# Performance work log

Hardware: AMD Instinct MI355X
Metric: run time of the kernel (lower is better)

Reference implementation:

```python
import jax, jax.numpy as jnp
import numpy as np

PAD = 1
DIL = 1
K = 9  # 3x3 kernel points


def conv2d(x, w, b):
    # standard NCHW conv, stride 1, padding PAD, dilation DIL
    y = jax.lax.conv_general_dilated(
        x, w, window_strides=(1, 1), padding=[(PAD, PAD), (PAD, PAD)],
        rhs_dilation=(DIL, DIL), dimension_numbers=('NCHW', 'OIHW', 'NCHW'))
    return y + b[None, :, None, None]


def deform_conv(x, offset, w):
    # x: [B,C,H,W], offset: [B,2K,H,W] (y at 2k, x at 2k+1), w: [O,C,3,3]
    B, C, H, W = x.shape
    O = w.shape[0]
    off = offset.reshape(B, K, 2, H, W)
    ky = jnp.repeat(jnp.arange(3), 3).astype(x.dtype)  # [K]
    kx = jnp.tile(jnp.arange(3), 3).astype(x.dtype)    # [K]
    base_h = jnp.arange(H, dtype=x.dtype) - PAD
    base_w = jnp.arange(W, dtype=x.dtype) - PAD
    # sampling positions [B,K,H,W]
    py = base_h[None, None, :, None] + (ky * DIL)[None, :, None, None] + off[:, :, 0]
    px = base_w[None, None, None, :] + (kx * DIL)[None, :, None, None] + off[:, :, 1]
    y0 = jnp.floor(py)
    x0 = jnp.floor(px)
    wy = py - y0
    wx = px - x0

    def gather(yi, xi):
        yc = jnp.clip(yi, 0, H - 1).astype(jnp.int32)
        xc = jnp.clip(xi, 0, W - 1).astype(jnp.int32)
        valid = ((yi >= 0) & (yi <= H - 1) & (xi >= 0) & (xi <= W - 1)).astype(x.dtype)
        # per-batch fancy gather -> [B,C,K,H,W]
        v = jax.vmap(lambda xb, yb, xbb: xb[:, yb, xbb])(x, yc, xc)
        return v * valid[:, None]

    v00 = gather(y0, x0)
    v01 = gather(y0, x0 + 1)
    v10 = gather(y0 + 1, x0)
    v11 = gather(y0 + 1, x0 + 1)
    a = (1 - wy)[:, None]; b_ = wy[:, None]
    c = (1 - wx)[:, None]; d = wx[:, None]
    samp = v00 * a * c + v01 * a * d + v10 * b_ * c + v11 * b_ * d  # [B,C,K,H,W]
    return jnp.einsum('bckhw,ock->bohw', samp, w.reshape(O, C, K))


def layer(x, w_off, b_off, w):
    offset = conv2d(x, w_off, b_off)
    return jax.nn.relu(deform_conv(x, offset, w))


def setup_inputs() -> dict:
    key = jax.random.key(0)
    ks = jax.random.split(key, 10)
    B, C, H, W = 4, 256, 96, 96
    inp = {"x": jax.random.normal(ks[0], (B, C, H, W), jnp.float32)}
    s = 1.0 / np.sqrt(C * 9)  # kaiming-ish scale for deform weights
    for i in range(3):
        inp[f"w_off{i}"] = jax.random.normal(ks[1 + 3 * i], (2 * K, C, 3, 3), jnp.float32) * 0.01
        inp[f"b_off{i}"] = jnp.zeros((2 * K,), jnp.float32)
        inp[f"w{i}"] = jax.random.normal(ks[3 + 3 * i], (C, C, 3, 3), jnp.float32) * s
    return inp


def reference(x, w_off0, b_off0, w0, w_off1, b_off1, w1, w_off2, b_off2, w2):
    for (wo, bo, w) in ((w_off0, b_off0, w0), (w_off1, b_off1, w1), (w_off2, b_off2, w2)):
        x = layer(x, wo, bo, w)
    return x
```

## Files before the change

kernel.cpp:

```cpp
#include <hip/hip_runtime.h>

#define Hc 96
#define Wc 96
#define Cc 256
#define Bc 4
#define KK 9
#define HW 9216
#define PIX 36864
#define CK 2304

typedef _Float16 f16;
typedef __attribute__((ext_vector_type(4))) _Float16 f16x4;
typedef __attribute__((ext_vector_type(8))) _Float16 f16x8;
typedef __attribute__((ext_vector_type(4))) float f32x4;

__device__ __forceinline__ int clampi(int v, int lo, int hi) {
    return v < lo ? lo : (v > hi ? hi : v);
}

#define SB() __builtin_amdgcn_sched_barrier(0)

__global__ __launch_bounds__(256) void nhwc_prep_kernel(
    const float* __restrict__ x0, f16* __restrict__ x16)
{
    __shared__ float st[64][65];
    const int hw0 = blockIdx.x * 64;
    const int c0  = blockIdx.y * 64;
    const int b   = blockIdx.z;
    const int tid = threadIdx.x;
    const int a = tid & 63, r = tid >> 6;
#pragma unroll
    for (int it = 0; it < 16; ++it) {
        int cl = it * 4 + r;
        st[cl][a] = x0[((size_t)(b * Cc + c0 + cl)) * HW + hw0 + a];
    }
    __syncthreads();
#pragma unroll
    for (int it = 0; it < 16; ++it) {
        int hwl = it * 4 + r;
        x16[((size_t)(b * HW + hw0 + hwl)) * Cc + c0 + a] = (f16)st[a][hwl];
    }
}

__global__ __launch_bounds__(256) void wprep_kernel(
    const float* __restrict__ w, const float* __restrict__ w_off,
    f16* __restrict__ wT2, f16* __restrict__ woffT)
{
    int b = blockIdx.x;
    if (b < 2304) {
        int u = b * 256 + threadIdx.x;
        int c = u & 255, o = (u >> 8) & 255, k = u >> 16;
        wT2[u] = (f16)w[(o * Cc + c) * KK + k];
    } else {
        int u = (b - 2304) * 256 + threadIdx.x;
        int c = u & 255, j = (u >> 8) & 31, k = u >> 13;
        float v = (j < 18) ? w_off[((size_t)j * Cc + c) * KK + k] : 0.f;
        woffT[u] = (f16)v;
    }
}

__device__ __forceinline__ void store_tap(int k, int h, int w, float offy, float offx,
    int p, int4* __restrict__ idx4t, float4* __restrict__ wt4t)
{
    float py = (float)(h - 1 + k / 3) + offy;
    float px = (float)(w - 1 + k % 3) + offx;
    float y0f = floorf(py), x0f = floorf(px);
    float wy = py - y0f, wx = px - x0f;
    int iy0 = (int)y0f, ix0 = (int)x0f;
    float vy0 = (y0f >= 0.f && y0f <= 95.f) ? 1.f : 0.f;
    float vy1 = (y0f + 1.f >= 0.f && y0f + 1.f <= 95.f) ? 1.f : 0.f;
    float vx0 = (x0f >= 0.f && x0f <= 95.f) ? 1.f : 0.f;
    float vx1 = (x0f + 1.f >= 0.f && x0f + 1.f <= 95.f) ? 1.f : 0.f;
    int cy0 = clampi(iy0, 0, 95), cy1 = clampi(iy0 + 1, 0, 95);
    int cx0 = clampi(ix0, 0, 95), cx1 = clampi(ix0 + 1, 0, 95);
    idx4t[(size_t)k * PIX + p] = make_int4(cy0 * Wc + cx0, cy0 * Wc + cx1,
                                           cy1 * Wc + cx0, cy1 * Wc + cx1);
    wt4t[(size_t)k * PIX + p] = make_float4((1.f - wy) * (1.f - wx) * vy0 * vx0,
                                            (1.f - wy) * wx * vy0 * vx1,
                                            wy * (1.f - wx) * vy1 * vx0,
                                            wy * wx * vy1 * vx1);
}

__global__ __launch_bounds__(256) void conv_off_mfma_kernel(
    const f16* __restrict__ x16, const f16* __restrict__ woffT,
    const float* __restrict__ b_off,
    int4* __restrict__ idx4t, float4* __restrict__ wt4t)
{
    __shared__ __align__(16) f16 s_a[2][32 * 32];
    __shared__ __align__(16) f16 s_b[2][64 * 32];
    const int bid = blockIdx.x;
    const int swz = (bid & 7) * 72 + (bid >> 3);
    const int p0 = swz * 64;
    const int imgb = (p0 / HW) * HW;
    const int tid = threadIdx.x, lane = tid & 63, wid = tid >> 6;
    const int wm = wid >> 1, wn = wid & 1;
    const int qa = ((lane >> 4) ^ ((lane >> 1) & 3)) * 8;
    const int arow = tid >> 3, acb = tid & 7;
    const int adst = arow * 32 + (((acb >> 1) ^ ((arow >> 1) & 3)) * 8) + (acb & 1) * 4;
    const int ps = tid >> 2, cg = tid & 3;
    const int bdst = ps * 32 + ((cg ^ ((ps >> 1) & 3)) * 8);
    const int hwp = p0 + ps - imgb;
    const int hp = hwp / Wc, wp = hwp - hp * Wc;

#define CLOAD(q, aD, bD) do {                                                  \
    int p2_ = (q) > 71 ? 71 : (q);                                             \
    int k2_ = p2_ >> 3, c2_ = p2_ & 7;                                         \
    int ky_ = k2_ / 3, kx_ = k2_ - ky_ * 3;                                    \
    int yy_ = hp + ky_ - 1, xx_ = wp + kx_ - 1;                                \
    bool v_ = (yy_ >= 0 && yy_ < Hc && xx_ >= 0 && xx_ < Wc);                  \
    aD = *(const f16x4*)(woffT + ((size_t)(k2_ * 32 + arow)) * Cc + c2_ * 32 + acb * 4); \
    f16x8 t_ = {0, 0, 0, 0, 0, 0, 0, 0};                                       \
    if (v_) t_ = *(const f16x8*)(x16 + ((size_t)(imgb + yy_ * Wc + xx_)) * Cc + c2_ * 32 + cg * 8); \
    bD = t_;                                                                   \
} while (0)

    f32x4 acc[2];
    acc[0] = (f32x4){0.f, 0.f, 0.f, 0.f};
    acc[1] = (f32x4){0.f, 0.f, 0.f, 0.f};

    f16x4 aR0, aR1;
    f16x8 bR0, bR1;
    CLOAD(0, aR0, bR0);
    CLOAD(1, aR1, bR1);
    *(f16x4*)&s_a[0][adst] = aR0;
    *(f16x8*)&s_b[0][bdst] = bR0;
    asm volatile("s_waitcnt lgkmcnt(0)" ::: "memory"); SB();
    __builtin_amdgcn_s_barrier(); SB();

#define CBODY(p, aCur, bCur, aNxt, bNxt, bc, bn) do {                          \
    f16x8 af = *(const f16x8*)&s_a[bc][(wm * 16 + (lane & 15)) * 32 + qa];     \
    f16x8 bf0 = *(const f16x8*)&s_b[bc][(wn * 32 + (lane & 15)) * 32 + qa];    \
    f16x8 bf1 = *(const f16x8*)&s_b[bc][(wn * 32 + 16 + (lane & 15)) * 32 + qa];\
    CLOAD((p) + 2, aCur, bCur);                                                \
    acc[0] = __builtin_amdgcn_mfma_f32_16x16x32_f16(af, bf0, acc[0], 0, 0, 0); \
    acc[1] = __builtin_amdgcn_mfma_f32_16x16x32_f16(af, bf1, acc[1], 0, 0, 0); \
    *(f16x4*)&s_a[bn][adst] = aNxt;                                            \
    *(f16x8*)&s_b[bn][bdst] = bNxt;                                            \
    asm volatile("s_waitcnt lgkmcnt(0)" ::: "memory"); SB();                   \
    __builtin_amdgcn_s_barrier(); SB();                                        \
} while (0)

    for (int p = 0; p < 72; p += 2) {
        CBODY(p,     aR0, bR0, aR1, bR1, 0, 1);
        CBODY(p + 1, aR1, bR1, aR0, bR0, 1, 0);
    }

    const int g = lane >> 4;
#pragma unroll
    for (int ni = 0; ni < 2; ++ni) {
        const int p = p0 + wn * 32 + ni * 16 + (lane & 15);
        const int hwq = p - imgb;
        const int hq = hwq / Wc, wq = hwq - hq * Wc;
        if (wm == 0) {
            store_tap(2 * g,     hq, wq, acc[ni][0] + b_off[4 * g],
                                         acc[ni][1] + b_off[4 * g + 1], p, idx4t, wt4t);
            store_tap(2 * g + 1, hq, wq, acc[ni][2] + b_off[4 * g + 2],
                                         acc[ni][3] + b_off[4 * g + 3], p, idx4t, wt4t);
        } else if (g == 0) {
            store_tap(8, hq, wq, acc[ni][0] + b_off[16],
                                 acc[ni][1] + b_off[17], p, idx4t, wt4t);
        }
    }
#undef CLOAD
#undef CBODY
}

__global__ __launch_bounds__(768, 3) void deform_mfma_kernel(
    const f16* __restrict__ x16, const f16* __restrict__ wT2,
    const int4* __restrict__ idx4t, const float4* __restrict__ wt4t,
    f16* __restrict__ o16, float* __restrict__ oN, int last)
{
    __shared__ __align__(16) f16 s_w[2][2][8192];
    __shared__ __align__(16) f16 s_s[2][2][4608];

    const int bid = blockIdx.x;
    const int swz = (bid & 7) * 32 + (bid >> 3);
    const int p0 = swz * 144;
    const int imgb = (p0 / HW) * HW;
    const int tid = threadIdx.x, lane = tid & 63, wid = tid >> 6;
    const int wo = wid & 3, wp = wid >> 2;
    const bool sampler = (wid < 9);
    const int ps = tid >> 2, cg = tid & 3;
    const int qa = ((lane >> 4) ^ ((lane >> 1) & 3)) * 8;
    const int qs = (cg ^ ((ps >> 1) & 3)) * 8;
    const f16* xb = x16 + (size_t)imgb * Cc;
    const int wlo = (tid >> 2) * Cc + ((tid & 3) ^ ((tid >> 3) & 3)) * 8;
    const int wds = tid * 8;

#define ISSUE_W(kt, cq, h, nb) do {                                            \
    const f16* g0_ = wT2 + wlo + ((size_t)((kt) * 256)) * Cc + (cq) * 64 + (h) * 32; \
    __builtin_amdgcn_global_load_lds(                                          \
        (const __attribute__((address_space(1))) void*)g0_,                    \
        (__attribute__((address_space(3))) void*)&s_w[nb][h][wds], 16, 0, 0);  \
    if (wid >= 8) {                                                            \
        const f16* g1_ = wT2 + wlo + ((size_t)((kt) * 256 + 64)) * Cc + (cq) * 64 + (h) * 32; \
        __builtin_amdgcn_global_load_lds(                                      \
            (const __attribute__((address_space(1))) void*)g1_,                \
            (__attribute__((address_space(3))) void*)&s_w[nb][h][2048 + wds], 16, 0, 0); \
    }                                                                          \
} while (0)

#define ISSUE_C(dst, idv, co) do {                                             \
    (dst)[0] = *(const f16x8*)(xb + (size_t)(idv).x * Cc + (co) + cg * 8);     \
    (dst)[1] = *(const f16x8*)(xb + (size_t)(idv).y * Cc + (co) + cg * 8);     \
    (dst)[2] = *(const f16x8*)(xb + (size_t)(idv).z * Cc + (co) + cg * 8);     \
    (dst)[3] = *(const f16x8*)(xb + (size_t)(idv).w * Cc + (co) + cg * 8);     \
} while (0)

#define BLEND_WRITE(src, wvv, h, nb) do {                                      \
    f16x8 sv_ = (src)[0] * (f16)(wvv).x + (src)[1] * (f16)(wvv).y              \
              + (src)[2] * (f16)(wvv).z + (src)[3] * (f16)(wvv).w;             \
    *(f16x8*)&s_s[nb][h][ps * 32 + qs] = sv_;                                  \
} while (0)

    f32x4 acc[4][3];
#pragma unroll
    for (int mi = 0; mi < 4; ++mi)
#pragma unroll
        for (int ni = 0; ni < 3; ++ni) acc[mi][ni] = (f32x4){0.f, 0.f, 0.f, 0.f};

    f16x8 c4a[4], c4b[4];
    int4 id;
    float4 wv;
    int4 idN;
    float4 wvN;
    if (sampler) {
        id = idx4t[p0 + ps];
        wv = wt4t[p0 + ps];
    }

    ISSUE_W(0, 0, 0, 0);
    ISSUE_W(0, 0, 1, 0);
    SB();
    if (sampler) {
        ISSUE_C(c4a, id, 0);
        ISSUE_C(c4b, id, 32);
        BLEND_WRITE(c4a, wv, 0, 0);
        BLEND_WRITE(c4b, wv, 1, 0);
        ISSUE_C(c4a, id, 64);
        ISSUE_C(c4b, id, 96);
        asm volatile("s_waitcnt lgkmcnt(0)" ::: "memory"); SB();
        if (wid == 8) {
            asm volatile("s_waitcnt vmcnt(8)" ::: "memory"); SB();
        }
    } else {
        asm volatile("s_waitcnt vmcnt(0)" ::: "memory"); SB();
    }
    __builtin_amdgcn_s_barrier(); SB();

    for (int k = 0; k < 9; ++k) {
        const int kn = (k < 8) ? k + 1 : 8;
#pragma unroll
        for (int ch = 0; ch < 4; ++ch) {
            const int bb = ch & 1, nb = bb ^ 1;
            f16x8 bf0[3], bf1[3];
#pragma unroll
            for (int ni = 0; ni < 3; ++ni) {
                bf0[ni] = *(const f16x8*)&s_s[bb][0][(wp * 48 + ni * 16 + (lane & 15)) * 32 + qa];
                bf1[ni] = *(const f16x8*)&s_s[bb][1][(wp * 48 + ni * 16 + (lane & 15)) * 32 + qa];
            }
            if (sampler) {
                if (ch == 1) {
                    idN = idx4t[(size_t)kn * PIX + p0 + ps];
                    wvN = wt4t[(size_t)kn * PIX + p0 + ps];
                }
                ISSUE_W((ch == 3) ? kn : k, (ch + 1) & 3, 0, nb);
                ISSUE_W((ch == 3) ? kn : k, (ch + 1) & 3, 1, nb);
                SB();
                {
                    const float4 wvu = (ch == 3) ? wvN : wv;
                    const int4 idu = (ch >= 2) ? idN : id;
                    const int co2 = ((ch + 2) & 3) * 64;
                    BLEND_WRITE(c4a, wvu, 0, nb);
                    ISSUE_C(c4a, idu, co2);
                    BLEND_WRITE(c4b, wvu, 1, nb);
                    ISSUE_C(c4b, idu, co2 + 32);
                }
            } else {
                ISSUE_W((ch == 3) ? kn : k, (ch + 1) & 3, 0, nb);
                ISSUE_W((ch == 3) ? kn : k, (ch + 1) & 3, 1, nb);
                SB();
            }
#pragma unroll
            for (int mi = 0; mi < 4; ++mi) {
                f16x8 af = *(const f16x8*)&s_w[bb][0][(wo * 64 + mi * 16 + (lane & 15)) * 32 + qa];
#pragma unroll
                for (int ni = 0; ni < 3; ++ni)
                    acc[mi][ni] = __builtin_amdgcn_mfma_f32_16x16x32_f16(
                        af, bf0[ni], acc[mi][ni], 0, 0, 0);
            }
#pragma unroll
            for (int mi = 0; mi < 4; ++mi) {
                f16x8 af = *(const f16x8*)&s_w[bb][1][(wo * 64 + mi * 16 + (lane & 15)) * 32 + qa];
#pragma unroll
                for (int ni = 0; ni < 3; ++ni)
                    acc[mi][ni] = __builtin_amdgcn_mfma_f32_16x16x32_f16(
                        af, bf1[ni], acc[mi][ni], 0, 0, 0);
            }
            asm volatile("s_waitcnt lgkmcnt(0)" ::: "memory"); SB();
            if (sampler) {
                asm volatile("s_waitcnt vmcnt(8)" ::: "memory"); SB();
            } else {
                asm volatile("s_waitcnt vmcnt(0)" ::: "memory"); SB();
            }
            __builtin_amdgcn_s_barrier(); SB();
        }
        if (sampler) { id = idN; wv = wvN; }
    }

    if (!last) {
#pragma unroll
        for (int ni = 0; ni < 3; ++ni) {
            const int p = p0 + wp * 48 + ni * 16 + (lane & 15);
#pragma unroll
            for (int mi = 0; mi < 4; ++mi) {
                const int o0 = wo * 64 + mi * 16 + (lane >> 4) * 4;
                f32x4 v = acc[mi][ni];
                f16x4 h = {(f16)fmaxf(v[0], 0.f), (f16)fmaxf(v[1], 0.f),
                           (f16)fmaxf(v[2], 0.f), (f16)fmaxf(v[3], 0.f)};
                *(f16x4*)&o16[(size_t)p * Cc + o0] = h;
            }
        }
    } else {
        const int bimg = imgb / HW;
#pragma unroll
        for (int ni = 0; ni < 3; ++ni) {
            const int p = p0 + wp * 48 + ni * 16 + (lane & 15);
            const int hwl = p - imgb;
#pragma unroll
            for (int mi = 0; mi < 4; ++mi) {
                const int o0 = wo * 64 + mi * 16 + (lane >> 4) * 4;
#pragma unroll
                for (int j = 0; j < 4; ++j)
                    oN[((size_t)(bimg * Cc + o0 + j)) * HW + hwl] =
                        fmaxf(acc[mi][ni][j], 0.f);
            }
        }
    }
#undef ISSUE_W
#undef ISSUE_C
#undef BLEND_WRITE
}

extern "C" void kernel_launch(void* const* d_in, const int* in_sizes, int n_in,
                              void* d_out, int out_size, void* d_ws, size_t ws_size,
                              hipStream_t stream)
{
    const float* x0 = (const float*)d_in[0];
    float* out = (float*)d_out;

    f16*   x16a = (f16*)d_ws;
    f16*   x16b = x16a + (size_t)PIX * Cc;
    f16*   wT2  = x16b + (size_t)PIX * Cc;
    f16*   woffT = wT2 + (size_t)CK * Cc;
    int4*  idx4t = (int4*)(woffT + (size_t)9 * 32 * Cc);
    float4* wt4t = (float4*)(idx4t + (size_t)KK * PIX);

    nhwc_prep_kernel<<<dim3(HW / 64, Cc / 64, Bc), 256, 0, stream>>>(x0, x16a);

    const f16* xin = x16a;
    for (int L = 0; L < 3; ++L) {
        const float* w_off = (const float*)d_in[1 + 3 * L];
        const float* b_off = (const float*)d_in[2 + 3 * L];
        const float* w     = (const float*)d_in[3 + 3 * L];
        const int last = (L == 2);
        f16* xo = (L == 0) ? x16b : x16a;

        wprep_kernel<<<2592, 256, 0, stream>>>(w, w_off, wT2, woffT);
        conv_off_mfma_kernel<<<PIX / 64, 256, 0, stream>>>(xin, woffT, b_off, idx4t, wt4t);
        deform_mfma_kernel<<<PIX / 144, 768, 0, stream>>>(
            xin, wT2, idx4t, wt4t, xo, out, last);

        xin = xo;
    }
}
```

Measured before the change: 287.5 us.

## Fuse offset convolution into deform kernel and batch weight prep across layers

The offset-predicting 3x3 conv is computed inside the deform kernel's prologue with MFMA: sampler warps gather the x tile and loader warps stage the offset weights. The resulting bilinear indices and weights go to LDS instead of global buffers, which removes one kernel launch per layer and the idx/wt global round trip. Weight conversion for all three layers now runs in a single launch up front. The cost is extra LDS use, which may limit occupancy, and the offset GEMM runs at the block's 144-pixel granularity with only some warps busy, which could serialize the prologue.

```diff
diff --git a/kernel.cpp b/kernel.cpp
--- a/kernel.cpp
+++ b/kernel.cpp
@@ -42,136 +42,38 @@
     }
 }
 
-__global__ __launch_bounds__(256) void wprep_kernel(
-    const float* __restrict__ w, const float* __restrict__ w_off,
+__global__ __launch_bounds__(256) void wprep_all_kernel(
+    const float* __restrict__ w0, const float* __restrict__ wo0,
+    const float* __restrict__ w1, const float* __restrict__ wo1,
+    const float* __restrict__ w2, const float* __restrict__ wo2,
     f16* __restrict__ wT2, f16* __restrict__ woffT)
 {
-    int b = blockIdx.x;
+    int bb = blockIdx.x;
+    int l = bb / 2592, b = bb - l * 2592;
+    const float* w = (l == 0) ? w0 : (l == 1) ? w1 : w2;
+    const float* wo = (l == 0) ? wo0 : (l == 1) ? wo1 : wo2;
     if (b < 2304) {
         int u = b * 256 + threadIdx.x;
         int c = u & 255, o = (u >> 8) & 255, k = u >> 16;
-        wT2[u] = (f16)w[(o * Cc + c) * KK + k];
+        wT2[(size_t)l * CK * Cc + u] = (f16)w[(o * Cc + c) * KK + k];
     } else {
         int u = (b - 2304) * 256 + threadIdx.x;
         int c = u & 255, j = (u >> 8) & 31, k = u >> 13;
-        float v = (j < 18) ? w_off[((size_t)j * Cc + c) * KK + k] : 0.f;
-        woffT[u] = (f16)v;
-    }
-}
-
-__device__ __forceinline__ void store_tap(int k, int h, int w, float offy, float offx,
-    int p, int4* __restrict__ idx4t, float4* __restrict__ wt4t)
-{
-    float py = (float)(h - 1 + k / 3) + offy;
-    float px = (float)(w - 1 + k % 3) + offx;
-    float y0f = floorf(py), x0f = floorf(px);
-    float wy = py - y0f, wx = px - x0f;
-    int iy0 = (int)y0f, ix0 = (int)x0f;
-    float vy0 = (y0f >= 0.f && y0f <= 95.f) ? 1.f : 0.f;
-    float vy1 = (y0f + 1.f >= 0.f && y0f + 1.f <= 95.f) ? 1.f : 0.f;
-    float vx0 = (x0f >= 0.f && x0f <= 95.f) ? 1.f : 0.f;
-    float vx1 = (x0f + 1.f >= 0.f && x0f + 1.f <= 95.f) ? 1.f : 0.f;
-    int cy0 = clampi(iy0, 0, 95), cy1 = clampi(iy0 + 1, 0, 95);
-    int cx0 = clampi(ix0, 0, 95), cx1 = clampi(ix0 + 1, 0, 95);
-    idx4t[(size_t)k * PIX + p] = make_int4(cy0 * Wc + cx0, cy0 * Wc + cx1,
-                                           cy1 * Wc + cx0, cy1 * Wc + cx1);
-    wt4t[(size_t)k * PIX + p] = make_float4((1.f - wy) * (1.f - wx) * vy0 * vx0,
-                                            (1.f - wy) * wx * vy0 * vx1,
-                                            wy * (1.f - wx) * vy1 * vx0,
-                                            wy * wx * vy1 * vx1);
-}
-
-__global__ __launch_bounds__(256) void conv_off_mfma_kernel(
-    const f16* __restrict__ x16, const f16* __restrict__ woffT,
-    const float* __restrict__ b_off,
-    int4* __restrict__ idx4t, float4* __restrict__ wt4t)
-{
-    __shared__ __align__(16) f16 s_a[2][32 * 32];
-    __shared__ __align__(16) f16 s_b[2][64 * 32];
-    const int bid = blockIdx.x;
-    const int swz = (bid & 7) * 72 + (bid >> 3);
-    const int p0 = swz * 64;
-    const int imgb = (p0 / HW) * HW;
-    const int tid = threadIdx.x, lane = tid & 63, wid = tid >> 6;
-    const int wm = wid >> 1, wn = wid & 1;
-    const int qa = ((lane >> 4) ^ ((lane >> 1) & 3)) * 8;
-    const int arow = tid >> 3, acb = tid & 7;
-    const int adst = arow * 32 + (((acb >> 1) ^ ((arow >> 1) & 3)) * 8) + (acb & 1) * 4;
-    const int ps = tid >> 2, cg = tid & 3;
-    const int bdst = ps * 32 + ((cg ^ ((ps >> 1) & 3)) * 8);
-    const int hwp = p0 + ps - imgb;
-    const int hp = hwp / Wc, wp = hwp - hp * Wc;
-
-#define CLOAD(q, aD, bD) do {                                                  \
-    int p2_ = (q) > 71 ? 71 : (q);                                             \
-    int k2_ = p2_ >> 3, c2_ = p2_ & 7;                                         \
-    int ky_ = k2_ / 3, kx_ = k2_ - ky_ * 3;                                    \
-    int yy_ = hp + ky_ - 1, xx_ = wp + kx_ - 1;                                \
-    bool v_ = (yy_ >= 0 && yy_ < Hc && xx_ >= 0 && xx_ < Wc);                  \
-    aD = *(const f16x4*)(woffT + ((size_t)(k2_ * 32 + arow)) * Cc + c2_ * 32 + acb * 4); \
-    f16x8 t_ = {0, 0, 0, 0, 0, 0, 0, 0};                                       \
-    if (v_) t_ = *(const f16x8*)(x16 + ((size_t)(imgb + yy_ * Wc + xx_)) * Cc + c2_ * 32 + cg * 8); \
-    bD = t_;                                                                   \
-} while (0)
-
-    f32x4 acc[2];
-    acc[0] = (f32x4){0.f, 0.f, 0.f, 0.f};
-    acc[1] = (f32x4){0.f, 0.f, 0.f, 0.f};
-
-    f16x4 aR0, aR1;
-    f16x8 bR0, bR1;
-    CLOAD(0, aR0, bR0);
-    CLOAD(1, aR1, bR1);
-    *(f16x4*)&s_a[0][adst] = aR0;
-    *(f16x8*)&s_b[0][bdst] = bR0;
-    asm volatile("s_waitcnt lgkmcnt(0)" ::: "memory"); SB();
-    __builtin_amdgcn_s_barrier(); SB();
-
-#define CBODY(p, aCur, bCur, aNxt, bNxt, bc, bn) do {                          \
-    f16x8 af = *(const f16x8*)&s_a[bc][(wm * 16 + (lane & 15)) * 32 + qa];     \
-    f16x8 bf0 = *(const f16x8*)&s_b[bc][(wn * 32 + (lane & 15)) * 32 + qa];    \
-    f16x8 bf1 = *(const f16x8*)&s_b[bc][(wn * 32 + 16 + (lane & 15)) * 32 + qa];\
-    CLOAD((p) + 2, aCur, bCur);                                                \
-    acc[0] = __builtin_amdgcn_mfma_f32_16x16x32_f16(af, bf0, acc[0], 0, 0, 0); \
-    acc[1] = __builtin_amdgcn_mfma_f32_16x16x32_f16(af, bf1, acc[1], 0, 0, 0); \
-    *(f16x4*)&s_a[bn][adst] = aNxt;                                            \
-    *(f16x8*)&s_b[bn][bdst] = bNxt;                                            \
-    asm volatile("s_waitcnt lgkmcnt(0)" ::: "memory"); SB();                   \
-    __builtin_amdgcn_s_barrier(); SB();                                        \
-} while (0)
-
-    for (int p = 0; p < 72; p += 2) {
-        CBODY(p,     aR0, bR0, aR1, bR1, 0, 1);
-        CBODY(p + 1, aR1, bR1, aR0, bR0, 1, 0);
-    }
-
-    const int g = lane >> 4;
-#pragma unroll
-    for (int ni = 0; ni < 2; ++ni) {
-        const int p = p0 + wn * 32 + ni * 16 + (lane & 15);
-        const int hwq = p - imgb;
-        const int hq = hwq / Wc, wq = hwq - hq * Wc;
-        if (wm == 0) {
-            store_tap(2 * g,     hq, wq, acc[ni][0] + b_off[4 * g],
-                                         acc[ni][1] + b_off[4 * g + 1], p, idx4t, wt4t);
-            store_tap(2 * g + 1, hq, wq, acc[ni][2] + b_off[4 * g + 2],
-                                         acc[ni][3] + b_off[4 * g + 3], p, idx4t, wt4t);
-        } else if (g == 0) {
-            store_tap(8, hq, wq, acc[ni][0] + b_off[16],
-                                 acc[ni][1] + b_off[17], p, idx4t, wt4t);
-        }
-    }
-#undef CLOAD
-#undef CBODY
-}
-
-__global__ __launch_bounds__(768, 3) void deform_mfma_kernel(
+        float v = (j < 18) ? wo[((size_t)j * Cc + c) * KK + k] : 0.f;
+        woffT[(size_t)l * 9 * 32 * Cc + u] = (f16)v;
+    }
+}
+
+__global__ __launch_bounds__(768, 3) void fused_layer_kernel(
     const f16* __restrict__ x16, const f16* __restrict__ wT2,
-    const int4* __restrict__ idx4t, const float4* __restrict__ wt4t,
+    const f16* __restrict__ woffT, const float* __restrict__ b_off,
     f16* __restrict__ o16, float* __restrict__ oN, int last)
 {
     __shared__ __align__(16) f16 s_w[2][2][8192];
     __shared__ __align__(16) f16 s_s[2][2][4608];
+    __shared__ __align__(16) f16 s_a[2][2][1024];
+    __shared__ int4   s_id[9][144];
+    __shared__ float4 s_wt[9][144];
 
     const int bid = blockIdx.x;
     const int swz = (bid & 7) * 32 + (bid >> 3);
@@ -186,6 +88,114 @@
     const f16* xb = x16 + (size_t)imgb * Cc;
     const int wlo = (tid >> 2) * Cc + ((tid & 3) ^ ((tid >> 3) & 3)) * 8;
     const int wds = tid * 8;
+    const int hwp = p0 + ps - imgb;
+    const int hp = hwp / Wc, wp_ = hwp - hp * Wc;
+    const int au0 = tid - 576;
+    const int arow0 = au0 >> 3, acb0 = au0 & 7;
+    const int ah0 = acb0 >> 2, aq0 = acb0 & 3;
+    const int adst0 = arow0 * 32 + ((aq0 ^ ((arow0 >> 1) & 3)) * 8);
+    const int arow1 = arow0 + 24;
+    const int adst1 = arow1 * 32 + ((aq0 ^ ((arow1 >> 1) & 3)) * 8);
+
+    {
+        f32x4 accA[2];
+        accA[0] = (f32x4){0.f, 0.f, 0.f, 0.f};
+        accA[1] = (f32x4){0.f, 0.f, 0.f, 0.f};
+        f16x8 bR0, bR1, aR0, aR1;
+
+#define PA_LOAD(q) do {                                                        \
+    int q_ = (q) > 35 ? 35 : (q);                                              \
+    int k2_ = q_ >> 2, cq_ = q_ & 3;                                           \
+    int ky_ = k2_ / 3, kx_ = k2_ - ky_ * 3;                                    \
+    if (sampler) {                                                             \
+        int yy_ = hp + ky_ - 1, xx_ = wp_ + kx_ - 1;                           \
+        f16x8 t0_ = {0,0,0,0,0,0,0,0}, t1_ = {0,0,0,0,0,0,0,0};                \
+        if (yy_ >= 0 && yy_ < Hc && xx_ >= 0 && xx_ < Wc) {                    \
+            const f16* s_ = x16 + ((size_t)(imgb + yy_ * Wc + xx_)) * Cc + cq_ * 64 + cg * 8; \
+            t0_ = *(const f16x8*)s_;                                           \
+            t1_ = *(const f16x8*)(s_ + 32);                                    \
+        }                                                                      \
+        bR0 = t0_; bR1 = t1_;                                                  \
+    } else {                                                                   \
+        aR0 = *(const f16x8*)(woffT + ((size_t)(k2_ * 32 + arow0)) * Cc + cq_ * 64 + acb0 * 8); \
+        if (tid < 640)                                                         \
+            aR1 = *(const f16x8*)(woffT + ((size_t)(k2_ * 32 + arow1)) * Cc + cq_ * 64 + acb0 * 8); \
+    }                                                                          \
+} while (0)
+
+#define PA_STAGE(nb) do {                                                      \
+    if (sampler) {                                                             \
+        *(f16x8*)&s_s[nb][0][ps * 32 + qs] = bR0;                              \
+        *(f16x8*)&s_s[nb][1][ps * 32 + qs] = bR1;                              \
+    } else {                                                                   \
+        *(f16x8*)&s_a[nb][ah0][adst0] = aR0;                                   \
+        if (tid < 640) *(f16x8*)&s_a[nb][ah0][adst1] = aR1;                    \
+    }                                                                          \
+} while (0)
+
+        PA_LOAD(0);
+        PA_STAGE(0);
+        asm volatile("s_waitcnt lgkmcnt(0)" ::: "memory"); SB();
+        __builtin_amdgcn_s_barrier(); SB();
+
+        for (int p = 0; p < 36; ++p) {
+            const int bb = p & 1, nb = bb ^ 1;
+            f16x8 af0, af1, bf0, bf1;
+            if (sampler) {
+                af0 = *(const f16x8*)&s_a[bb][0][((lane & 15)) * 32 + qa];
+                af1 = *(const f16x8*)&s_a[bb][0][((16 + (lane & 15))) * 32 + qa];
+                bf0 = *(const f16x8*)&s_s[bb][0][(wid * 16 + (lane & 15)) * 32 + qa];
+            }
+            PA_LOAD(p + 1);
+            if (sampler) {
+                accA[0] = __builtin_amdgcn_mfma_f32_16x16x32_f16(af0, bf0, accA[0], 0, 0, 0);
+                accA[1] = __builtin_amdgcn_mfma_f32_16x16x32_f16(af1, bf0, accA[1], 0, 0, 0);
+                af0 = *(const f16x8*)&s_a[bb][1][((lane & 15)) * 32 + qa];
+                af1 = *(const f16x8*)&s_a[bb][1][((16 + (lane & 15))) * 32 + qa];
+                bf1 = *(const f16x8*)&s_s[bb][1][(wid * 16 + (lane & 15)) * 32 + qa];
+                accA[0] = __builtin_amdgcn_mfma_f32_16x16x32_f16(af0, bf1, accA[0], 0, 0, 0);
+                accA[1] = __builtin_amdgcn_mfma_f32_16x16x32_f16(af1, bf1, accA[1], 0, 0, 0);
+            }
+            PA_STAGE(nb);
+            asm volatile("s_waitcnt lgkmcnt(0)" ::: "memory"); SB();
+            __builtin_amdgcn_s_barrier(); SB();
+        }
+
+        if (sampler) {
+            const int q = lane >> 4;
+            const int pxl = wid * 16 + (lane & 15);
+            const int hwq = p0 + pxl - imgb;
+            const int hq = hwq / Wc, wq = hwq - hq * Wc;
+#define STORE_TAP_LDS(kk, offy, offx) do {                                     \
+    float py_ = (float)(hq - 1 + (kk) / 3) + (offy);                           \
+    float px_ = (float)(wq - 1 + (kk) % 3) + (offx);                           \
+    float y0f_ = floorf(py_), x0f_ = floorf(px_);                              \
+    float wy_ = py_ - y0f_, wx_ = px_ - x0f_;                                  \
+    int iy0_ = (int)y0f_, ix0_ = (int)x0f_;                                    \
+    float vy0_ = (y0f_ >= 0.f && y0f_ <= 95.f) ? 1.f : 0.f;                    \
+    float vy1_ = (y0f_ + 1.f >= 0.f && y0f_ + 1.f <= 95.f) ? 1.f : 0.f;        \
+    float vx0_ = (x0f_ >= 0.f && x0f_ <= 95.f) ? 1.f : 0.f;                    \
+    float vx1_ = (x0f_ + 1.f >= 0.f && x0f_ + 1.f <= 95.f) ? 1.f : 0.f;        \
+    int cy0_ = clampi(iy0_, 0, 95), cy1_ = clampi(iy0_ + 1, 0, 95);            \
+    int cx0_ = clampi(ix0_, 0, 95), cx1_ = clampi(ix0_ + 1, 0, 95);            \
+    s_id[kk][pxl] = make_int4(cy0_ * Wc + cx0_, cy0_ * Wc + cx1_,              \
+                              cy1_ * Wc + cx0_, cy1_ * Wc + cx1_);             \
+    s_wt[kk][pxl] = make_float4((1.f - wy_) * (1.f - wx_) * vy0_ * vx0_,       \
+                                (1.f - wy_) * wx_ * vy0_ * vx1_,               \
+                                wy_ * (1.f - wx_) * vy1_ * vx0_,               \
+                                wy_ * wx_ * vy1_ * vx1_);                      \
+} while (0)
+            STORE_TAP_LDS(2 * q,     accA[0][0] + b_off[4 * q],
+                                     accA[0][1] + b_off[4 * q + 1]);
+            STORE_TAP_LDS(2 * q + 1, accA[0][2] + b_off[4 * q + 2],
+                                     accA[0][3] + b_off[4 * q + 3]);
+            if (q == 0)
+                STORE_TAP_LDS(8, accA[1][0] + b_off[16], accA[1][1] + b_off[17]);
+#undef STORE_TAP_LDS
+        }
+        asm volatile("s_waitcnt lgkmcnt(0)" ::: "memory"); SB();
+        __builtin_amdgcn_s_barrier(); SB();
+    }
 
 #define ISSUE_W(kt, cq, h, nb) do {                                            \
     const f16* g0_ = wT2 + wlo + ((size_t)((kt) * 256)) * Cc + (cq) * 64 + (h) * 32; \
@@ -225,8 +235,8 @@
     int4 idN;
     float4 wvN;
     if (sampler) {
-        id = idx4t[p0 + ps];
-        wv = wt4t[p0 + ps];
+        id = s_id[0][ps];
+        wv = s_wt[0][ps];
     }
 
     ISSUE_W(0, 0, 0, 0);
@@ -261,8 +271,8 @@
             }
             if (sampler) {
                 if (ch == 1) {
-                    idN = idx4t[(size_t)kn * PIX + p0 + ps];
-                    wvN = wt4t[(size_t)kn * PIX + p0 + ps];
+                    idN = s_id[kn][ps];
+                    wvN = s_wt[kn][ps];
                 }
                 ISSUE_W((ch == 3) ? kn : k, (ch + 1) & 3, 0, nb);
                 ISSUE_W((ch == 3) ? kn : k, (ch + 1) & 3, 1, nb);
@@ -340,6 +350,8 @@
 #undef ISSUE_W
 #undef ISSUE_C
 #undef BLEND_WRITE
+#undef PA_LOAD
+#undef PA_STAGE
 }
 
 extern "C" void kernel_launch(void* const* d_in, const int* in_sizes, int n_in,
@@ -352,24 +364,24 @@
     f16*   x16a = (f16*)d_ws;
     f16*   x16b = x16a + (size_t)PIX * Cc;
     f16*   wT2  = x16b + (size_t)PIX * Cc;
-    f16*   woffT = wT2 + (size_t)CK * Cc;
-    int4*  idx4t = (int4*)(woffT + (size_t)9 * 32 * Cc);
-    float4* wt4t = (float4*)(idx4t + (size_t)KK * PIX);
+    f16*   woffT = wT2 + (size_t)3 * CK * Cc;
 
     nhwc_prep_kernel<<<dim3(HW / 64, Cc / 64, Bc), 256, 0, stream>>>(x0, x16a);
+    wprep_all_kernel<<<3 * 2592, 256, 0, stream>>>(
+        (const float*)d_in[3], (const float*)d_in[1],
+        (const float*)d_in[6], (const float*)d_in[4],
+        (const float*)d_in[9], (const float*)d_in[7],
+        wT2, woffT);
 
     const f16* xin = x16a;
     for (int L = 0; L < 3; ++L) {
-        const float* w_off = (const float*)d_in[1 + 3 * L];
         const float* b_off = (const float*)d_in[2 + 3 * L];
-        const float* w     = (const float*)d_in[3 + 3 * L];
         const int last = (L == 2);
         f16* xo = (L == 0) ? x16b : x16a;
 
-        wprep_kernel<<<2592, 256, 0, stream>>>(w, w_off, wT2, woffT);
-        conv_off_mfma_kernel<<<PIX / 64, 256, 0, stream>>>(xin, woffT, b_off, idx4t, wt4t);
-        deform_mfma_kernel<<<PIX / 144, 768, 0, stream>>>(
-            xin, wT2, idx4t, wt4t, xo, out, last);
+        fused_layer_kernel<<<PIX / 144, 768, 0, stream>>>(
+            xin, wT2 + (size_t)L * CK * Cc, woffT + (size_t)L * 9 * 32 * Cc,
+            b_off, xo, out, last);
 
         xin = xo;
     }
```

Measured after the change: 258.2 us. 10.2% less time.
